# Kernel optimization log

Hardware: AMD Instinct MI355X
Metric: run time of the kernel (lower is better)

## Reference

```python
import jax, jax.numpy as jnp
import numpy as np

B, S, M_DIM, N_DIM, K_NNZ = 8, 2048, 2048, 2048, 205


def setup_inputs() -> dict:
    key = jax.random.key(0)
    k1, k2, k3, k4 = jax.random.split(key, 4)
    x = jax.random.normal(k1, (B, S, M_DIM), dtype=jnp.float32)
    # CSR structure: K_NNZ unique, sorted column indices per row
    scores = jax.random.uniform(k2, (N_DIM, M_DIM))
    cols = jnp.sort(jnp.argsort(scores, axis=1)[:, :K_NNZ], axis=1)  # [N, K] unique per row
    indices = cols.reshape(-1).astype(jnp.int32)                      # [nnz]
    indptr = (jnp.arange(N_DIM + 1) * K_NNZ).astype(jnp.int32)        # [N+1]
    W_val = jax.random.normal(k3, (N_DIM * K_NNZ,), dtype=jnp.float32) * (1.0 / np.sqrt(M_DIM))
    bias = jax.random.normal(k4, (N_DIM,), dtype=jnp.float32) * 0.01
    return {"x": x, "W_val": W_val, "bias": bias, "indices": indices, "indptr": indptr}


def reference(x, W_val, bias, indices, indptr):
    # SparseLinear.forward: y = x @ W^T + bias, with W stored in CSR
    # (W_val: nnz values, indptr: [N+1] row pointers, indices: [nnz] column ids).
    N = indptr.shape[0] - 1
    M = x.shape[-1]
    nnz = W_val.shape[0]
    # row id of each nonzero, derived from indptr (standard CSR expansion)
    row_ids = jnp.searchsorted(indptr, jnp.arange(nnz, dtype=indptr.dtype), side="right") - 1
    # materialize the sparse weight (CSR columns are unique per row -> set is exact)
    W = jnp.zeros((N, M), dtype=W_val.dtype).at[row_ids, indices].set(W_val)
    return jnp.einsum("bsm,nm->bsn", x, W) + bias
```

## Files before the change

kernel.cpp:

```cpp
#include <hip/hip_runtime.h>
#include <hip/hip_bf16.h>
#include <stdint.h>

#define B_DIM 8
#define S_DIM 2048
#define M_TOT 16384
#define K_TOT 2048
#define N_TOT 2048

#define BM 128
#define BN 128
#define BK 32

typedef __attribute__((ext_vector_type(8))) short short8;
typedef __attribute__((ext_vector_type(4))) float float4v;
typedef __attribute__((ext_vector_type(8))) unsigned short ushort8;

__device__ __forceinline__ unsigned short f2bf(float f) {
    union { float f; unsigned u; } a; a.f = f;
    unsigned r = a.u + 0x7FFFu + ((a.u >> 16) & 1u);
    return (unsigned short)(r >> 16);
}

__global__ void cast_x_kernel(const float* __restrict__ x, unsigned short* __restrict__ xb) {
    int i = blockIdx.x * blockDim.x + threadIdx.x;
    const float4* xf = (const float4*)x;
    float4 a = xf[2 * i];
    float4 b = xf[2 * i + 1];
    ushort8 o;
    o[0] = f2bf(a.x); o[1] = f2bf(a.y); o[2] = f2bf(a.z); o[3] = f2bf(a.w);
    o[4] = f2bf(b.x); o[5] = f2bf(b.y); o[6] = f2bf(b.z); o[7] = f2bf(b.w);
    ((ushort8*)xb)[i] = o;
}

__global__ void zero_kernel(float4* __restrict__ p) {
    int i = blockIdx.x * blockDim.x + threadIdx.x;
    p[i] = float4{0.f, 0.f, 0.f, 0.f};
}

__global__ void scatter_kernel(const float* __restrict__ val, const int* __restrict__ idx,
                               const int* __restrict__ indptr, unsigned short* __restrict__ Wb) {
    int n = blockIdx.x;
    int s = indptr[n], e = indptr[n + 1];
    for (int j = s + threadIdx.x; j < e; j += blockDim.x) {
        Wb[(size_t)n * K_TOT + idx[j]] = f2bf(val[j]);
    }
}

__global__ __launch_bounds__(256) void gemm_bias_kernel(
    const unsigned short* __restrict__ A,
    const unsigned short* __restrict__ Bw,
    const float* __restrict__ bias,
    float* __restrict__ C)
{
    __shared__ unsigned short Asm[BM * BK];
    __shared__ unsigned short Bsm[BN * BK];

    const int tid  = threadIdx.x;
    const int lane = tid & 63;
    const int wave = tid >> 6;
    const int bm = blockIdx.y;
    const int bn = blockIdx.x;

    const int srow   = wave * 16 + (lane >> 2);
    const int schunk = (lane & 3) * 8;

    const unsigned short* a_g0 = A  + (size_t)(bm * BM + srow) * K_TOT + schunk;
    const unsigned short* a_g1 = a_g0 + (size_t)64 * K_TOT;
    const unsigned short* b_g0 = Bw + (size_t)(bn * BN + srow) * K_TOT + schunk;
    const unsigned short* b_g1 = b_g0 + (size_t)64 * K_TOT;

    unsigned short* a_l0 = Asm + (wave * 16) * BK;
    unsigned short* a_l1 = Asm + (64 + wave * 16) * BK;
    unsigned short* b_l0 = Bsm + (wave * 16) * BK;
    unsigned short* b_l1 = Bsm + (64 + wave * 16) * BK;

    const int wm = (wave >> 1) * 64;
    const int wn = (wave & 1) * 64;
    const int mrow = lane & 15;
    const int quad = lane >> 4;

    float4v acc[4][4] = {};

    for (int k0 = 0; k0 < K_TOT; k0 += BK) {
        __syncthreads();
        __builtin_amdgcn_global_load_lds(
            (const __attribute__((address_space(1))) unsigned int*)(a_g0 + k0),
            (__attribute__((address_space(3))) unsigned int*)a_l0, 16, 0, 0);
        __builtin_amdgcn_global_load_lds(
            (const __attribute__((address_space(1))) unsigned int*)(a_g1 + k0),
            (__attribute__((address_space(3))) unsigned int*)a_l1, 16, 0, 0);
        __builtin_amdgcn_global_load_lds(
            (const __attribute__((address_space(1))) unsigned int*)(b_g0 + k0),
            (__attribute__((address_space(3))) unsigned int*)b_l0, 16, 0, 0);
        __builtin_amdgcn_global_load_lds(
            (const __attribute__((address_space(1))) unsigned int*)(b_g1 + k0),
            (__attribute__((address_space(3))) unsigned int*)b_l1, 16, 0, 0);
        __syncthreads();

        short8 af[4], bf_[4];
#pragma unroll
        for (int mi = 0; mi < 4; ++mi)
            af[mi] = *(const short8*)(Asm + (wm + mi * 16 + mrow) * BK + quad * 8);
#pragma unroll
        for (int ni = 0; ni < 4; ++ni)
            bf_[ni] = *(const short8*)(Bsm + (wn + ni * 16 + mrow) * BK + quad * 8);

#pragma unroll
        for (int mi = 0; mi < 4; ++mi)
#pragma unroll
            for (int ni = 0; ni < 4; ++ni)
                acc[mi][ni] = __builtin_amdgcn_mfma_f32_16x16x32_bf16(
                    af[mi], bf_[ni], acc[mi][ni], 0, 0, 0);
    }

#pragma unroll
    for (int ni = 0; ni < 4; ++ni) {
        const int col = bn * BN + wn + ni * 16 + mrow;
        const float bv = bias[col];
#pragma unroll
        for (int mi = 0; mi < 4; ++mi) {
#pragma unroll
            for (int r = 0; r < 4; ++r) {
                const int row = bm * BM + wm + mi * 16 + quad * 4 + r;
                C[(size_t)row * N_TOT + col] = acc[mi][ni][r] + bv;
            }
        }
    }
}

extern "C" void kernel_launch(void* const* d_in, const int* in_sizes, int n_in,
                              void* d_out, int out_size, void* d_ws, size_t ws_size,
                              hipStream_t stream) {
    const float* x      = (const float*)d_in[0];
    const float* W_val  = (const float*)d_in[1];
    const float* bias   = (const float*)d_in[2];
    const int*   indices = (const int*)d_in[3];
    const int*   indptr  = (const int*)d_in[4];
    float* out = (float*)d_out;

    unsigned short* xb = (unsigned short*)d_ws;
    unsigned short* Wb = xb + (size_t)M_TOT * K_TOT;
    if (ws_size < ((size_t)M_TOT * K_TOT + (size_t)N_TOT * K_TOT) * sizeof(unsigned short))
        return;

    cast_x_kernel<<<16384, 256, 0, stream>>>(x, xb);
    zero_kernel<<<2048, 256, 0, stream>>>((float4*)Wb);
    scatter_kernel<<<N_TOT, 256, 0, stream>>>(W_val, indices, indptr, Wb);
    dim3 grid(N_TOT / BN, M_TOT / BM);
    gemm_bias_kernel<<<grid, 256, 0, stream>>>(xb, Wb, bias, out);
}
```

Before: 392.5 us.

## Fuse fp32-to-bf16 cast of x into GEMM loads and merge W zero/scatter

Drops the separate pass that casts x to bf16. The GEMM now streams fp32 x tiles straight into LDS and converts them to bf16 (round-half-up via perm) while building MFMA fragments. The zero and scatter kernels become one per-row build kernel, and XOR swizzles are added to the LDS layouts of A and B to reduce bank conflicts. In exchange, the GEMM reads twice as many bytes for A on every N-tile and spends extra VALU work on conversion in the inner loop. The rounding also changes slightly from round-to-nearest-even to round-half-up.

Result: slower. 460.8 us (+17.4%).

```diff
diff --git a/kernel.cpp b/kernel.cpp
--- a/kernel.cpp
+++ b/kernel.cpp
@@ -2,8 +2,6 @@
 #include <hip/hip_bf16.h>
 #include <stdint.h>
 
-#define B_DIM 8
-#define S_DIM 2048
 #define M_TOT 16384
 #define K_TOT 2048
 #define N_TOT 2048
@@ -16,44 +14,36 @@
 typedef __attribute__((ext_vector_type(4))) float float4v;
 typedef __attribute__((ext_vector_type(8))) unsigned short ushort8;
 
-__device__ __forceinline__ unsigned short f2bf(float f) {
+__device__ __forceinline__ unsigned short f2bf_rne(float f) {
     union { float f; unsigned u; } a; a.f = f;
     unsigned r = a.u + 0x7FFFu + ((a.u >> 16) & 1u);
     return (unsigned short)(r >> 16);
 }
 
-__global__ void cast_x_kernel(const float* __restrict__ x, unsigned short* __restrict__ xb) {
-    int i = blockIdx.x * blockDim.x + threadIdx.x;
-    const float4* xf = (const float4*)x;
-    float4 a = xf[2 * i];
-    float4 b = xf[2 * i + 1];
-    ushort8 o;
-    o[0] = f2bf(a.x); o[1] = f2bf(a.y); o[2] = f2bf(a.z); o[3] = f2bf(a.w);
-    o[4] = f2bf(b.x); o[5] = f2bf(b.y); o[6] = f2bf(b.z); o[7] = f2bf(b.w);
-    ((ushort8*)xb)[i] = o;
+__device__ __forceinline__ unsigned pack2_bf16(float lo, float hi) {
+    union { float f; unsigned u; } a, b; a.f = lo; b.f = hi;
+    return __builtin_amdgcn_perm(b.u + 0x8000u, a.u + 0x8000u, 0x07060302u);
 }
 
-__global__ void zero_kernel(float4* __restrict__ p) {
-    int i = blockIdx.x * blockDim.x + threadIdx.x;
-    p[i] = float4{0.f, 0.f, 0.f, 0.f};
-}
-
-__global__ void scatter_kernel(const float* __restrict__ val, const int* __restrict__ idx,
+__global__ void build_w_kernel(const float* __restrict__ val, const int* __restrict__ idx,
                                const int* __restrict__ indptr, unsigned short* __restrict__ Wb) {
-    int n = blockIdx.x;
-    int s = indptr[n], e = indptr[n + 1];
-    for (int j = s + threadIdx.x; j < e; j += blockDim.x) {
-        Wb[(size_t)n * K_TOT + idx[j]] = f2bf(val[j]);
-    }
+    const int n = blockIdx.x;
+    unsigned short* row = Wb + (size_t)n * K_TOT;
+    ushort8 z = {0, 0, 0, 0, 0, 0, 0, 0};
+    ((ushort8*)row)[threadIdx.x] = z;
+    __syncthreads();
+    const int s = indptr[n], e = indptr[n + 1];
+    for (int j = s + (int)threadIdx.x; j < e; j += (int)blockDim.x)
+        row[idx[j]] = f2bf_rne(val[j]);
 }
 
 __global__ __launch_bounds__(256) void gemm_bias_kernel(
-    const unsigned short* __restrict__ A,
+    const float* __restrict__ X,
     const unsigned short* __restrict__ Bw,
     const float* __restrict__ bias,
     float* __restrict__ C)
 {
-    __shared__ unsigned short Asm[BM * BK];
+    __shared__ float          Asm[BM * BK];
     __shared__ unsigned short Bsm[BN * BK];
 
     const int tid  = threadIdx.x;
@@ -62,18 +52,26 @@
     const int bm = blockIdx.y;
     const int bn = blockIdx.x;
 
-    const int srow   = wave * 16 + (lane >> 2);
-    const int schunk = (lane & 3) * 8;
-
-    const unsigned short* a_g0 = A  + (size_t)(bm * BM + srow) * K_TOT + schunk;
-    const unsigned short* a_g1 = a_g0 + (size_t)64 * K_TOT;
-    const unsigned short* b_g0 = Bw + (size_t)(bn * BN + srow) * K_TOT + schunk;
-    const unsigned short* b_g1 = b_g0 + (size_t)64 * K_TOT;
-
-    unsigned short* a_l0 = Asm + (wave * 16) * BK;
-    unsigned short* a_l1 = Asm + (64 + wave * 16) * BK;
-    unsigned short* b_l0 = Bsm + (wave * 16) * BK;
-    unsigned short* b_l1 = Bsm + (64 + wave * 16) * BK;
+    const int a_row_l = lane >> 3;
+    const int a_chk   = ((lane & 7) ^ a_row_l) * 4;
+    const float* a_g[4];
+    float* a_l[4];
+#pragma unroll
+    for (int l = 0; l < 4; ++l) {
+        const int row = wave * 32 + l * 8 + a_row_l;
+        a_g[l] = X + (size_t)(bm * BM + row) * K_TOT + a_chk;
+        a_l[l] = Asm + (wave * 32 + l * 8) * BK;
+    }
+    const int b_row_l = lane >> 2;
+    const int b_chk   = ((lane & 3) ^ ((lane >> 3) & 3)) * 8;
+    const unsigned short* b_g[2];
+    unsigned short* b_l[2];
+#pragma unroll
+    for (int l = 0; l < 2; ++l) {
+        const int row = l * 64 + wave * 16 + b_row_l;
+        b_g[l] = Bw + (size_t)(bn * BN + row) * K_TOT + b_chk;
+        b_l[l] = Bsm + (l * 64 + wave * 16) * BK;
+    }
 
     const int wm = (wave >> 1) * 64;
     const int wn = (wave & 1) * 64;
@@ -84,27 +82,39 @@
 
     for (int k0 = 0; k0 < K_TOT; k0 += BK) {
         __syncthreads();
-        __builtin_amdgcn_global_load_lds(
-            (const __attribute__((address_space(1))) unsigned int*)(a_g0 + k0),
-            (__attribute__((address_space(3))) unsigned int*)a_l0, 16, 0, 0);
-        __builtin_amdgcn_global_load_lds(
-            (const __attribute__((address_space(1))) unsigned int*)(a_g1 + k0),
-            (__attribute__((address_space(3))) unsigned int*)a_l1, 16, 0, 0);
-        __builtin_amdgcn_global_load_lds(
-            (const __attribute__((address_space(1))) unsigned int*)(b_g0 + k0),
-            (__attribute__((address_space(3))) unsigned int*)b_l0, 16, 0, 0);
-        __builtin_amdgcn_global_load_lds(
-            (const __attribute__((address_space(1))) unsigned int*)(b_g1 + k0),
-            (__attribute__((address_space(3))) unsigned int*)b_l1, 16, 0, 0);
+#pragma unroll
+        for (int l = 0; l < 4; ++l)
+            __builtin_amdgcn_global_load_lds(
+                (const __attribute__((address_space(1))) unsigned int*)(a_g[l] + k0),
+                (__attribute__((address_space(3))) unsigned int*)a_l[l], 16, 0, 0);
+#pragma unroll
+        for (int l = 0; l < 2; ++l)
+            __builtin_amdgcn_global_load_lds(
+                (const __attribute__((address_space(1))) unsigned int*)(b_g[l] + k0),
+                (__attribute__((address_space(3))) unsigned int*)b_l[l], 16, 0, 0);
         __syncthreads();
 
         short8 af[4], bf_[4];
 #pragma unroll
-        for (int mi = 0; mi < 4; ++mi)
-            af[mi] = *(const short8*)(Asm + (wm + mi * 16 + mrow) * BK + quad * 8);
+        for (int mi = 0; mi < 4; ++mi) {
+            const int r  = wm + mi * 16 + mrow;
+            const int rx = r & 7;
+            const float4v* base = (const float4v*)(Asm + r * BK);
+            float4v p = base[(quad * 2) ^ rx];
+            float4v q = base[(quad * 2 + 1) ^ rx];
+            union { unsigned u[4]; short8 s; } cv;
+            cv.u[0] = pack2_bf16(p[0], p[1]);
+            cv.u[1] = pack2_bf16(p[2], p[3]);
+            cv.u[2] = pack2_bf16(q[0], q[1]);
+            cv.u[3] = pack2_bf16(q[2], q[3]);
+            af[mi] = cv.s;
+        }
 #pragma unroll
-        for (int ni = 0; ni < 4; ++ni)
-            bf_[ni] = *(const short8*)(Bsm + (wn + ni * 16 + mrow) * BK + quad * 8);
+        for (int ni = 0; ni < 4; ++ni) {
+            const int r = wn + ni * 16 + mrow;
+            const short8* base = (const short8*)(Bsm + r * BK);
+            bf_[ni] = base[quad ^ ((r >> 1) & 3)];
+        }
 
 #pragma unroll
         for (int mi = 0; mi < 4; ++mi)
@@ -132,21 +142,18 @@
 extern "C" void kernel_launch(void* const* d_in, const int* in_sizes, int n_in,
                               void* d_out, int out_size, void* d_ws, size_t ws_size,
                               hipStream_t stream) {
-    const float* x      = (const float*)d_in[0];
-    const float* W_val  = (const float*)d_in[1];
-    const float* bias   = (const float*)d_in[2];
+    const float* x       = (const float*)d_in[0];
+    const float* W_val   = (const float*)d_in[1];
+    const float* bias    = (const float*)d_in[2];
     const int*   indices = (const int*)d_in[3];
     const int*   indptr  = (const int*)d_in[4];
     float* out = (float*)d_out;
 
-    unsigned short* xb = (unsigned short*)d_ws;
-    unsigned short* Wb = xb + (size_t)M_TOT * K_TOT;
-    if (ws_size < ((size_t)M_TOT * K_TOT + (size_t)N_TOT * K_TOT) * sizeof(unsigned short))
+    unsigned short* Wb = (unsigned short*)d_ws;
+    if (ws_size < (size_t)N_TOT * K_TOT * sizeof(unsigned short))
         return;
 
-    cast_x_kernel<<<16384, 256, 0, stream>>>(x, xb);
-    zero_kernel<<<2048, 256, 0, stream>>>((float4*)Wb);
-    scatter_kernel<<<N_TOT, 256, 0, stream>>>(W_val, indices, indptr, Wb);
+    build_w_kernel<<<N_TOT, 256, 0, stream>>>(W_val, indices, indptr, Wb);
     dim3 grid(N_TOT / BN, M_TOT / BM);
-    gemm_bias_kernel<<<grid, 256, 0, stream>>>(xb, Wb, bias, out);
+    gemm_bias_kernel<<<grid, 256, 0, stream>>>(x, Wb, bias, out);
 }
```
